# Performance work log

Hardware: AMD Instinct MI355X
Metric: run time of the kernel (lower is better)

## Reference

```python
import jax, jax.numpy as jnp
import numpy as np

MEME_DIM = 64
NUM_NODES = 8192
VISION_NUM_MEMES = 2048
INPUTS_PER_NODE = 32
VOCAB_SIZE = 256
SOFT_CLIP = 3.0
SHARPNESS = 2.0


def setup_inputs() -> dict:
    key = jax.random.key(0)
    k1, k2, k3, k4 = jax.random.split(key, 4)
    x = jax.random.normal(k1, (VISION_NUM_MEMES, MEME_DIM), dtype=jnp.float32)
    memes_last = jax.random.normal(k2, (NUM_NODES, MEME_DIM), dtype=jnp.float32)
    input_indices = jax.random.randint(
        k3, (NUM_NODES, INPUTS_PER_NODE), 0, NUM_NODES + VISION_NUM_MEMES
    )
    vocab = jax.random.normal(k4, (NUM_NODES, MEME_DIM, VOCAB_SIZE), dtype=jnp.float32)
    raw_soft_clip = jnp.log(jnp.array([SOFT_CLIP], dtype=jnp.float32))
    raw_sharpness = jnp.log(jnp.array([SHARPNESS], dtype=jnp.float32))
    return {
        'x': x,
        'memes_last': memes_last,
        'input_indices': input_indices,
        'vocab': vocab,
        'raw_soft_clip': raw_soft_clip,
        'raw_sharpness': raw_sharpness,
    }


def _dot_products_to_fractions(d, soft_clip, sharpness):
    # standardize per node over vocab dim (torch .std is unbiased -> ddof=1)
    d = d - d.mean(axis=1, keepdims=True)
    d = d / (d.std(axis=1, keepdims=True, ddof=1) + 0.001)
    d = jnp.tanh(d / soft_clip) * soft_clip          # soft clip
    d = sharpness ** d                               # power sharpness
    return d / (d.sum(axis=1, keepdims=True) + 0.001)


def reference(x, memes_last, input_indices, vocab, raw_soft_clip, raw_sharpness):
    # concat vision memes with last-tick node memes: [(V+N), E]
    cat = jnp.concatenate([x, memes_last], axis=0)
    # spread: gather [N,K,E], mean over K, global standardize (scalar mean/std)
    g = cat[input_indices].mean(axis=1)              # [N, E]
    g = g - g.mean()
    g = g / g.std(ddof=1)
    # remix: per-node routing over vocab
    dot_products = jnp.einsum('ne,nev->nv', g, vocab)  # [N, V]
    soft_clip = jnp.exp(raw_soft_clip)               # [1]
    sharpness = jnp.exp(raw_sharpness)               # [1]
    fractions = _dot_products_to_fractions(dot_products, soft_clip, sharpness)
    return jnp.einsum('nev,nv->ne', vocab, fractions)  # [N, E]
```

## Files before the change

kernel.cpp:

```cpp
#include <hip/hip_runtime.h>
#include <hip/hip_bf16.h>

#define N_NODES 8192
#define DIM 64
#define VIS 2048
#define KIN 32
#define VOC 256

typedef unsigned short u16;

__device__ __forceinline__ float bf2f(u16 u) {
    union { unsigned int i; float f; } c; c.i = ((unsigned int)u) << 16; return c.f;
}
__device__ __forceinline__ u16 f2bf(float f) {
    union { float f; unsigned int i; } c; c.f = f;
    unsigned int r = c.i + 0x7fffu + ((c.i >> 16) & 1u);
    return (u16)(r >> 16);
}
__device__ __forceinline__ float bflo(unsigned int w) {
    union { unsigned int i; float f; } c; c.i = w << 16; return c.f;
}
__device__ __forceinline__ float bfhi(unsigned int w) {
    union { unsigned int i; float f; } c; c.i = w & 0xffff0000u; return c.f;
}

__global__ __launch_bounds__(256) void k_gather(
    const float* __restrict__ x, const float* __restrict__ memes,
    const int* __restrict__ idx, float* __restrict__ graw,
    float* __restrict__ part)
{
    int tid  = threadIdx.x;
    int wid  = tid >> 6;
    int lane = tid & 63;
    int n = blockIdx.x * 4 + wid;
    const int* irow = idx + n * KIN;

    float acc = 0.f;
#pragma unroll
    for (int k = 0; k < KIN; ++k) {
        int id = irow[k];
        const float* row = (id < VIS) ? (x + (size_t)id * DIM)
                                      : (memes + (size_t)(id - VIS) * DIM);
        acc += row[lane];
    }
    float g = acc * (1.0f / KIN);
    graw[(size_t)n * DIM + lane] = g;

    float s = g, q = g * g;
#pragma unroll
    for (int m = 32; m >= 1; m >>= 1) {
        s += __shfl_xor(s, m, 64);
        q += __shfl_xor(q, m, 64);
    }
    __shared__ float sh[8];
    if (lane == 0) { sh[wid] = s; sh[wid + 4] = q; }
    __syncthreads();
    if (tid == 0) {
        part[blockIdx.x * 2 + 0] = sh[0] + sh[1] + sh[2] + sh[3];
        part[blockIdx.x * 2 + 1] = sh[4] + sh[5] + sh[6] + sh[7];
    }
}

__global__ __launch_bounds__(1024) void k_stats(
    const float* __restrict__ part, float* __restrict__ scal)
{
    int tid = threadIdx.x;
    float s = 0.f, q = 0.f;
    for (int i = tid; i < 2048; i += 1024) {
        s += part[2 * i];
        q += part[2 * i + 1];
    }
#pragma unroll
    for (int m = 32; m >= 1; m >>= 1) {
        s += __shfl_xor(s, m, 64);
        q += __shfl_xor(q, m, 64);
    }
    __shared__ float sh[32];
    int wid = tid >> 6, lane = tid & 63;
    if (lane == 0) { sh[wid] = s; sh[wid + 16] = q; }
    __syncthreads();
    if (tid == 0) {
        float S = 0.f, Q = 0.f;
#pragma unroll
        for (int i = 0; i < 16; ++i) { S += sh[i]; Q += sh[i + 16]; }
        const float M = (float)(N_NODES * DIM);
        float mean = S / M;
        float var  = (Q - S * S / M) / (M - 1.0f);
        scal[0] = mean;
        scal[1] = 1.0f / sqrtf(var);
    }
}

__global__ __launch_bounds__(256, 4) void k_remix(
    const float* __restrict__ vocab, const float* __restrict__ graw,
    const float* __restrict__ scal,
    const float* __restrict__ rclip, const float* __restrict__ rsharp,
    float* __restrict__ out)
{
    __shared__ __align__(16) u16 vs[DIM * VOC];
    __shared__ __align__(16) float dpart[4 * VOC];
    __shared__ float p_s[VOC];
    __shared__ float red_s[VOC];
    __shared__ float sh[8];

    const int tid = threadIdx.x;
    const int n = blockIdx.x;
    const int wid = tid >> 6, lane = tid & 63;

    const float mean = scal[0], istd = scal[1];
    const float gme = (graw[(size_t)n * DIM + lane] - mean) * istd;

    const float4* vb4 = (const float4*)(vocab + (size_t)n * (DIM * VOC));
    ushort4* vs4 = (ushort4*)vs;

    float d0 = 0.f, d1 = 0.f, d2 = 0.f, d3 = 0.f;
#pragma unroll
    for (int b = 0; b < 2; ++b) {
        float4 w[8];
#pragma unroll
        for (int i = 0; i < 8; ++i)
            w[i] = vb4[(b * 8 + i) * 256 + tid];
#pragma unroll
        for (int i = 0; i < 8; ++i) {
            const int ii = b * 8 + i;
            const float ge = __shfl(gme, 4 * ii + wid, 64);
            d0 = fmaf(ge, w[i].x, d0);
            d1 = fmaf(ge, w[i].y, d1);
            d2 = fmaf(ge, w[i].z, d2);
            d3 = fmaf(ge, w[i].w, d3);
            ushort4 h;
            h.x = f2bf(w[i].x); h.y = f2bf(w[i].y);
            h.z = f2bf(w[i].z); h.w = f2bf(w[i].w);
            vs4[ii * 256 + tid] = h;
        }
    }
    float4 dp; dp.x = d0; dp.y = d1; dp.z = d2; dp.w = d3;
    *(float4*)&dpart[wid * VOC + lane * 4] = dp;
    __syncthreads();

    float d = dpart[0 * VOC + tid] + dpart[1 * VOC + tid]
            + dpart[2 * VOC + tid] + dpart[3 * VOC + tid];

    float s = d, q = d * d;
#pragma unroll
    for (int m = 32; m >= 1; m >>= 1) {
        s += __shfl_xor(s, m, 64);
        q += __shfl_xor(q, m, 64);
    }
    if (lane == 0) { sh[wid] = s; sh[wid + 4] = q; }
    __syncthreads();
    float S = sh[0] + sh[1] + sh[2] + sh[3];
    float Q = sh[4] + sh[5] + sh[6] + sh[7];
    float mD  = S * (1.0f / VOC);
    float var = (Q - S * S * (1.0f / VOC)) * (1.0f / (VOC - 1));
    float sdD = sqrtf(fmaxf(var, 0.f));

    float clip = expf(rclip[0]);
    float l2s  = rsharp[0] * 1.44269504088896f;

    float dn = (d - mD) / (sdD + 0.001f);
    float tt = tanhf(dn / clip) * clip;
    float p  = exp2f(tt * l2s);
    p_s[tid] = p;

    float ps = p;
#pragma unroll
    for (int m = 32; m >= 1; m >>= 1) ps += __shfl_xor(ps, m, 64);
    __syncthreads();
    if (lane == 0) sh[wid] = ps;
    __syncthreads();
    float invden = 1.0f / (sh[0] + sh[1] + sh[2] + sh[3] + 0.001f);

    const int e = tid >> 2, qd = tid & 3;
    const u16* row = vs + e * VOC + qd * 64;
    const float* pp = p_s + qd * 64;
    const int i0 = e & 7;
    float acc = 0.f;
#pragma unroll
    for (int k = 0; k < 8; ++k) {
        int i = (i0 + k) & 7;
        uint4 w = *(const uint4*)(row + i * 8);
        const float* pj = pp + i * 8;
        acc = fmaf(bflo(w.x), pj[0], acc);
        acc = fmaf(bfhi(w.x), pj[1], acc);
        acc = fmaf(bflo(w.y), pj[2], acc);
        acc = fmaf(bfhi(w.y), pj[3], acc);
        acc = fmaf(bflo(w.z), pj[4], acc);
        acc = fmaf(bfhi(w.z), pj[5], acc);
        acc = fmaf(bflo(w.w), pj[6], acc);
        acc = fmaf(bfhi(w.w), pj[7], acc);
    }
    red_s[tid] = acc;
    __syncthreads();
    if (tid < DIM) {
        const float4 r = *(const float4*)&red_s[tid * 4];
        out[(size_t)n * DIM + tid] = (r.x + r.y + r.z + r.w) * invden;
    }
}

extern "C" void kernel_launch(void* const* d_in, const int* in_sizes, int n_in,
                              void* d_out, int out_size, void* d_ws, size_t ws_size,
                              hipStream_t stream)
{
    const float* x      = (const float*)d_in[0];
    const float* memes  = (const float*)d_in[1];
    const int*   idx    = (const int*)d_in[2];
    const float* vocab  = (const float*)d_in[3];
    const float* rclip  = (const float*)d_in[4];
    const float* rsharp = (const float*)d_in[5];
    float* out = (float*)d_out;

    float* scal = (float*)d_ws;
    float* part = (float*)((char*)d_ws + 64);
    float* graw = (float*)((char*)d_ws + 32768);

    k_gather<<<N_NODES / 4, 256, 0, stream>>>(x, memes, idx, graw, part);
    k_stats<<<1, 1024, 0, stream>>>(part, scal);
    k_remix<<<N_NODES, 256, 0, stream>>>(vocab, graw, scal, rclip, rsharp, out);
}
```

Measured before the change: 693.2 us.

## Keep bf16-packed vocab tile in registers instead of shared memory in remix

The remix kernel no longer stages the bf16-converted vocab tile in a 32KB shared array. Each thread keeps its 16 float4 chunks packed as bf16 pairs in registers and computes the second einsum with per-row wave shuffle reductions. Launch bounds go from 4 to 6 blocks per CU. This cuts LDS traffic and footprint to raise occupancy for the memory-bound vocab stream, at the cost of 16 shuffle reductions (6 steps each) per thread and higher register pressure.

```diff
diff --git a/kernel.cpp b/kernel.cpp
--- a/kernel.cpp
+++ b/kernel.cpp
@@ -8,20 +8,17 @@
 #define VOC 256
 
 typedef unsigned short u16;
+typedef unsigned int u32;
 
-__device__ __forceinline__ float bf2f(u16 u) {
-    union { unsigned int i; float f; } c; c.i = ((unsigned int)u) << 16; return c.f;
+__device__ __forceinline__ float bflo(u32 w) {
+    union { u32 i; float f; } c; c.i = w << 16; return c.f;
 }
-__device__ __forceinline__ u16 f2bf(float f) {
-    union { float f; unsigned int i; } c; c.f = f;
-    unsigned int r = c.i + 0x7fffu + ((c.i >> 16) & 1u);
-    return (u16)(r >> 16);
+__device__ __forceinline__ float bfhi(u32 w) {
+    union { u32 i; float f; } c; c.i = w & 0xffff0000u; return c.f;
 }
-__device__ __forceinline__ float bflo(unsigned int w) {
-    union { unsigned int i; float f; } c; c.i = w << 16; return c.f;
-}
-__device__ __forceinline__ float bfhi(unsigned int w) {
-    union { unsigned int i; float f; } c; c.i = w & 0xffff0000u; return c.f;
+__device__ __forceinline__ u32 pk_bf16(float a, float b) {
+    __hip_bfloat162 h = __float22bfloat162_rn(make_float2(a, b));
+    u32 u; __builtin_memcpy(&u, &h, 4); return u;
 }
 
 __global__ __launch_bounds__(256) void k_gather(
@@ -91,16 +88,15 @@
     }
 }
 
-__global__ __launch_bounds__(256, 4) void k_remix(
+__global__ __launch_bounds__(256, 6) void k_remix(
     const float* __restrict__ vocab, const float* __restrict__ graw,
     const float* __restrict__ scal,
     const float* __restrict__ rclip, const float* __restrict__ rsharp,
     float* __restrict__ out)
 {
-    __shared__ __align__(16) u16 vs[DIM * VOC];
     __shared__ __align__(16) float dpart[4 * VOC];
-    __shared__ float p_s[VOC];
-    __shared__ float red_s[VOC];
+    __shared__ __align__(16) float p_s[VOC];
+    __shared__ float red_s[DIM];
     __shared__ float sh[8];
 
     const int tid = threadIdx.x;
@@ -111,28 +107,19 @@
     const float gme = (graw[(size_t)n * DIM + lane] - mean) * istd;
 
     const float4* vb4 = (const float4*)(vocab + (size_t)n * (DIM * VOC));
-    ushort4* vs4 = (ushort4*)vs;
 
+    u32 pkx[16], pky[16];
     float d0 = 0.f, d1 = 0.f, d2 = 0.f, d3 = 0.f;
 #pragma unroll
-    for (int b = 0; b < 2; ++b) {
-        float4 w[8];
-#pragma unroll
-        for (int i = 0; i < 8; ++i)
-            w[i] = vb4[(b * 8 + i) * 256 + tid];
-#pragma unroll
-        for (int i = 0; i < 8; ++i) {
-            const int ii = b * 8 + i;
-            const float ge = __shfl(gme, 4 * ii + wid, 64);
-            d0 = fmaf(ge, w[i].x, d0);
-            d1 = fmaf(ge, w[i].y, d1);
-            d2 = fmaf(ge, w[i].z, d2);
-            d3 = fmaf(ge, w[i].w, d3);
-            ushort4 h;
-            h.x = f2bf(w[i].x); h.y = f2bf(w[i].y);
-            h.z = f2bf(w[i].z); h.w = f2bf(w[i].w);
-            vs4[ii * 256 + tid] = h;
-        }
+    for (int i = 0; i < 16; ++i) {
+        float4 w = vb4[i * 256 + tid];
+        const float ge = __shfl(gme, 4 * i + wid, 64);
+        d0 = fmaf(ge, w.x, d0);
+        d1 = fmaf(ge, w.y, d1);
+        d2 = fmaf(ge, w.z, d2);
+        d3 = fmaf(ge, w.w, d3);
+        pkx[i] = pk_bf16(w.x, w.y);
+        pky[i] = pk_bf16(w.z, w.w);
     }
     float4 dp; dp.x = d0; dp.y = d1; dp.z = d2; dp.w = d3;
     *(float4*)&dpart[wid * VOC + lane * 4] = dp;
@@ -171,31 +158,19 @@
     __syncthreads();
     float invden = 1.0f / (sh[0] + sh[1] + sh[2] + sh[3] + 0.001f);
 
-    const int e = tid >> 2, qd = tid & 3;
-    const u16* row = vs + e * VOC + qd * 64;
-    const float* pp = p_s + qd * 64;
-    const int i0 = e & 7;
-    float acc = 0.f;
+    const float4 pv = *(const float4*)&p_s[lane * 4];
 #pragma unroll
-    for (int k = 0; k < 8; ++k) {
-        int i = (i0 + k) & 7;
-        uint4 w = *(const uint4*)(row + i * 8);
-        const float* pj = pp + i * 8;
-        acc = fmaf(bflo(w.x), pj[0], acc);
-        acc = fmaf(bfhi(w.x), pj[1], acc);
-        acc = fmaf(bflo(w.y), pj[2], acc);
-        acc = fmaf(bfhi(w.y), pj[3], acc);
-        acc = fmaf(bflo(w.z), pj[4], acc);
-        acc = fmaf(bfhi(w.z), pj[5], acc);
-        acc = fmaf(bflo(w.w), pj[6], acc);
-        acc = fmaf(bfhi(w.w), pj[7], acc);
+    for (int i = 0; i < 16; ++i) {
+        float a = fmaf(bflo(pkx[i]), pv.x,
+                  fmaf(bfhi(pkx[i]), pv.y,
+                  fmaf(bflo(pky[i]), pv.z,
+                       bfhi(pky[i]) * pv.w)));
+#pragma unroll
+        for (int m = 32; m >= 1; m >>= 1) a += __shfl_xor(a, m, 64);
+        if (lane == 0) red_s[4 * i + wid] = a;
     }
-    red_s[tid] = acc;
     __syncthreads();
-    if (tid < DIM) {
-        const float4 r = *(const float4*)&red_s[tid * 4];
-        out[(size_t)n * DIM + tid] = (r.x + r.y + r.z + r.w) * invden;
-    }
+    if (tid < DIM) out[(size_t)n * DIM + tid] = red_s[tid] * invden;
 }
 
 extern "C" void kernel_launch(void* const* d_in, const int* in_sizes, int n_in,
```

After: 708.2 us. 2.2% more time.
